# Performance work log

Measured on AMD Instinct MI355X. Metric: run time of the kernel, lower is better.

The kernel has to match this reference:

```python
import jax, jax.numpy as jnp
import numpy as np

B, C, Lc, Vc = 16, 8, 30, 10000
Lp, Vp = 64, 2000
N_IV = 128
BETA_C = 0.7
BETA_P = 0.7


def setup_inputs() -> dict:
    key = jax.random.key(0)
    ks = jax.random.split(key, 9)
    pred_captions = jax.random.normal(ks[0], (B, C, Lc, Vc), jnp.float32)
    gt_captions = jax.random.randint(ks[1], (B, C, Lc), 0, Vc)
    gt_cap_lens = jax.random.randint(ks[2], (B, C), 1, Lc + 1).astype(jnp.int32)
    gt_caps_count = jax.random.randint(ks[3], (B,), 1, C + 1).astype(jnp.int32)
    pred_program = jax.random.normal(ks[4], (B, Lp, Vp), jnp.float32)
    gt_program = jax.random.randint(ks[5], (B, Lp), 0, Vp)
    gt_prog_len = jax.random.randint(ks[6], (B,), 1, Lp + 1).astype(jnp.int32)
    # intervals [N,2,1]: sort along dim 1 so end >= start (well-conditioned union)
    pred_intervals = jnp.sort(jax.random.uniform(ks[7], (N_IV, 2, 1), jnp.float32), axis=1)
    gt_intervals = jnp.sort(jax.random.uniform(ks[8], (N_IV, 2, 1), jnp.float32), axis=1)
    scores = jnp.ones((3,), jnp.float32)  # config.combination_scores
    return dict(gt_captions=gt_captions, gt_cap_lens=gt_cap_lens,
                pred_captions=pred_captions, gt_program=gt_program,
                gt_prog_len=gt_prog_len, pred_program=pred_program,
                gt_intervals=gt_intervals, pred_intervals=pred_intervals,
                gt_caps_count=gt_caps_count, scores=scores)


def _sentlen_loss(logits, targets, lens, item_mask, beta):
    """SentenceLengthLoss ('mean'): -sum_t logsoftmax[t, tgt_t] / len_i**beta, / n_items.
    logits [..., T, V]; targets [..., T] int; lens [...] int; item_mask [...] bool.
    Masked form is exactly equivalent to the torch ragged gather/concat packing.
    """
    T = logits.shape[-2]
    tok_mask = (jnp.arange(T) < lens[..., None]) & item_mask[..., None]  # [..., T]
    logp = jax.nn.log_softmax(logits, axis=-1)
    tok_lp = jnp.take_along_axis(logp, targets[..., None], axis=-1)[..., 0]  # [..., T]
    w = jnp.where(item_mask,
                  1.0 / jnp.maximum(lens, 1).astype(jnp.float32) ** beta,
                  0.0)  # per-sentence weight 1/len**beta
    loss_sum = -jnp.sum(w[..., None] * jnp.where(tok_mask, tok_lp, 0.0))
    n_items = jnp.sum(item_mask.astype(jnp.float32))
    return loss_sum / n_items


def _iou_loss(pred_iv, gt_iv):
    # pred_iv, gt_iv: [N, 2, 1] (start, end)
    p0, p1 = pred_iv[:, 0, 0], pred_iv[:, 1, 0]
    g0, g1 = gt_iv[:, 0, 0], gt_iv[:, 1, 0]
    inter = jnp.clip(jnp.minimum(p1, g1) - jnp.maximum(p0, g0), 0.0)
    union = jnp.maximum(p1, g1) - jnp.minimum(p0, g0)
    return 1.0 - jnp.sum(inter / union) / pred_iv.shape[0]


def reference(gt_captions, gt_cap_lens, pred_captions, gt_program, gt_prog_len,
              pred_program, gt_intervals, pred_intervals, gt_caps_count, scores):
    # captions: caption i of video j is active iff i < gt_caps_count[j]
    cap_item_mask = jnp.arange(pred_captions.shape[1])[None, :] < gt_caps_count[:, None]
    cap_loss = _sentlen_loss(pred_captions, gt_captions, gt_cap_lens,
                             cap_item_mask, BETA_C)
    # program: one sequence per batch element, all active
    prog_item_mask = jnp.ones((pred_program.shape[0],), bool)
    prog_loss = _sentlen_loss(pred_program, gt_program, gt_prog_len,
                              prog_item_mask, BETA_P)
    iou_loss = _iou_loss(pred_intervals, gt_intervals)
    losses = jnp.stack([cap_loss, prog_loss, iou_loss])
    loss = jnp.sum(scores * losses)
    return (loss, cap_loss, prog_loss, iou_loss)
```

## Files before the change

### kernel.cpp

```cpp
#include <hip/hip_runtime.h>
#include <math.h>

#define B   16
#define C   8
#define LC  30
#define VC  10000
#define LP  64
#define VP  2000
#define N_IV 128
#define BETA 0.7f

constexpr int CAP_ROWS    = B * C * LC;
constexpr int PROG_ROWS   = B * LP;
constexpr int PROG_BLOCKS = PROG_ROWS / 4;
constexpr int N4C = VC / 4;
constexpr int KC  = (N4C + 255) / 256;
constexpr int N4P = VP / 4;
constexpr int KP  = (N4P + 63) / 64;

__global__ __launch_bounds__(256) void rows_kernel(
    const float* __restrict__ pred_cap,  const int* __restrict__ gt_cap,
    const int*  __restrict__ cap_lens,   const int* __restrict__ caps_count,
    const float* __restrict__ pred_prog, const int* __restrict__ gt_prog,
    const int*  __restrict__ prog_len,
    float* __restrict__ cap_part, float* __restrict__ prog_part)
{
    __shared__ float sred[4];
    __shared__ float ssum[4];

    const int bid = blockIdx.x;
    const int tid = threadIdx.x;

    if (bid < CAP_ROWS) {
        const int b   = bid / (C * LC);
        const int rem = bid % (C * LC);
        const int c   = rem / LC;
        const int t   = rem % LC;
        const int len = cap_lens[b * C + c];
        if (c >= caps_count[b] || t >= len) {
            if (tid == 0) cap_part[bid] = 0.0f;
            return;
        }
        const float*  row  = pred_cap + (size_t)bid * VC;
        const float4* row4 = (const float4*)row;

        float4 v[KC];
        #pragma unroll
        for (int k = 0; k < KC; k++) {
            const int j = tid + k * 256;
            if (j < N4C) v[k] = row4[j];
            else v[k] = make_float4(-INFINITY, -INFINITY, -INFINITY, -INFINITY);
        }

        float m = -INFINITY;
        #pragma unroll
        for (int k = 0; k < KC; k++)
            m = fmaxf(m, fmaxf(fmaxf(v[k].x, v[k].y), fmaxf(v[k].z, v[k].w)));
        #pragma unroll
        for (int off = 32; off; off >>= 1) m = fmaxf(m, __shfl_xor(m, off, 64));

        const int wid = tid >> 6;
        if ((tid & 63) == 0) sred[wid] = m;
        __syncthreads();
        const float M = fmaxf(fmaxf(sred[0], sred[1]), fmaxf(sred[2], sred[3]));

        float s = 0.0f;
        #pragma unroll
        for (int k = 0; k < KC; k++)
            s += __expf(v[k].x - M) + __expf(v[k].y - M)
               + __expf(v[k].z - M) + __expf(v[k].w - M);
        #pragma unroll
        for (int off = 32; off; off >>= 1) s += __shfl_xor(s, off, 64);

        if ((tid & 63) == 0) ssum[wid] = s;
        __syncthreads();

        if (tid == 0) {
            const float S   = ssum[0] + ssum[1] + ssum[2] + ssum[3];
            const float lse = M + logf(S);
            const float w   = powf((float)len, -BETA);
            cap_part[bid] = -w * (row[gt_cap[bid]] - lse);
        }
    } else {
        const int pb   = bid - CAP_ROWS;
        const int lane = tid & 63;
        const int wid  = tid >> 6;
        const int r    = pb * 4 + wid;
        const int b    = r / LP;
        const int t    = r % LP;
        const int len  = prog_len[b];
        if (t >= len) {
            if (lane == 0) prog_part[r] = 0.0f;
            return;
        }
        const float*  row  = pred_prog + (size_t)r * VP;
        const float4* row4 = (const float4*)row;

        float4 v[KP];
        #pragma unroll
        for (int k = 0; k < KP; k++) {
            const int j = lane + k * 64;
            if (j < N4P) v[k] = row4[j];
            else v[k] = make_float4(-INFINITY, -INFINITY, -INFINITY, -INFINITY);
        }

        float m = -INFINITY;
        #pragma unroll
        for (int k = 0; k < KP; k++)
            m = fmaxf(m, fmaxf(fmaxf(v[k].x, v[k].y), fmaxf(v[k].z, v[k].w)));
        #pragma unroll
        for (int off = 32; off; off >>= 1) m = fmaxf(m, __shfl_xor(m, off, 64));

        float s = 0.0f;
        #pragma unroll
        for (int k = 0; k < KP; k++)
            s += __expf(v[k].x - m) + __expf(v[k].y - m)
               + __expf(v[k].z - m) + __expf(v[k].w - m);
        #pragma unroll
        for (int off = 32; off; off >>= 1) s += __shfl_xor(s, off, 64);

        if (lane == 0) {
            const float lse = m + logf(s);
            const float w   = powf((float)len, -BETA);
            prog_part[r] = -w * (row[gt_prog[r]] - lse);
        }
    }
}

__device__ inline float wave_sum(float v) {
    #pragma unroll
    for (int off = 32; off; off >>= 1) v += __shfl_xor(v, off, 64);
    return v;
}

__global__ __launch_bounds__(256) void finish_kernel(
    const float* __restrict__ cap_part, const float* __restrict__ prog_part,
    const int*  __restrict__ caps_count,
    const float* __restrict__ pred_iv, const float* __restrict__ gt_iv,
    const float* __restrict__ scores, float* __restrict__ out)
{
    const int tid = threadIdx.x;

    float cs = 0.0f;
    for (int i = tid; i < CAP_ROWS; i += 256) cs += cap_part[i];
    float ps = 0.0f;
    for (int i = tid; i < PROG_ROWS; i += 256) ps += prog_part[i];

    float is = 0.0f;
    if (tid < N_IV) {
        const float p0 = pred_iv[tid * 2 + 0];
        const float p1 = pred_iv[tid * 2 + 1];
        const float g0 = gt_iv[tid * 2 + 0];
        const float g1 = gt_iv[tid * 2 + 1];
        const float inter = fmaxf(fminf(p1, g1) - fmaxf(p0, g0), 0.0f);
        const float uni   = fmaxf(p1, g1) - fminf(p0, g0);
        is = inter / uni;
    }

    float nc = 0.0f;
    if (tid < B) nc = (float)caps_count[tid];

    cs = wave_sum(cs);
    ps = wave_sum(ps);
    is = wave_sum(is);
    nc = wave_sum(nc);

    __shared__ float red[4][4];
    const int wid = tid >> 6;
    if ((tid & 63) == 0) {
        red[0][wid] = cs; red[1][wid] = ps; red[2][wid] = is; red[3][wid] = nc;
    }
    __syncthreads();

    if (tid == 0) {
        const float CS = red[0][0] + red[0][1] + red[0][2] + red[0][3];
        const float PS = red[1][0] + red[1][1] + red[1][2] + red[1][3];
        const float IS = red[2][0] + red[2][1] + red[2][2] + red[2][3];
        const float NC = red[3][0] + red[3][1] + red[3][2] + red[3][3];

        const float cap_loss  = CS / NC;
        const float prog_loss = PS / (float)B;
        const float iou_loss  = 1.0f - IS / (float)N_IV;
        const float loss = scores[0] * cap_loss + scores[1] * prog_loss
                         + scores[2] * iou_loss;
        out[0] = loss;
        out[1] = cap_loss;
        out[2] = prog_loss;
        out[3] = iou_loss;
    }
}

extern "C" void kernel_launch(void* const* d_in, const int* in_sizes, int n_in,
                              void* d_out, int out_size, void* d_ws, size_t ws_size,
                              hipStream_t stream) {
    const int*   gt_captions    = (const int*)  d_in[0];
    const int*   gt_cap_lens    = (const int*)  d_in[1];
    const float* pred_captions  = (const float*)d_in[2];
    const int*   gt_program     = (const int*)  d_in[3];
    const int*   gt_prog_len    = (const int*)  d_in[4];
    const float* pred_program   = (const float*)d_in[5];
    const float* gt_intervals   = (const float*)d_in[6];
    const float* pred_intervals = (const float*)d_in[7];
    const int*   gt_caps_count  = (const int*)  d_in[8];
    const float* scores         = (const float*)d_in[9];
    float* out = (float*)d_out;

    float* cap_part  = (float*)d_ws;
    float* prog_part = cap_part + CAP_ROWS;

    rows_kernel<<<CAP_ROWS + PROG_BLOCKS, 256, 0, stream>>>(
        pred_captions, gt_captions, gt_cap_lens, gt_caps_count,
        pred_program, gt_program, gt_prog_len,
        cap_part, prog_part);

    finish_kernel<<<1, 256, 0, stream>>>(
        cap_part, prog_part, gt_caps_count,
        pred_intervals, gt_intervals, scores, out);
}
```

Before: 22.77 us.

## Split caption rows into per-wave halves and merge partial softmax in finish kernel

Each caption row is now split into two halves, and a single wavefront computes each half's max and sum-exp. This drops the block-level shared-memory reductions and both __syncthreads. The finish kernel merges the two partial (m, s) pairs per row, gathers the target logit, and applies the length weight. The target-logit gather and weight math move into the single-block finish kernel, which adds serial work there. Fast-math __logf/__expf also replace logf/powf.

```diff
diff --git a/kernel.cpp b/kernel.cpp
--- a/kernel.cpp
+++ b/kernel.cpp
@@ -11,91 +11,81 @@
 #define BETA 0.7f
 
 constexpr int CAP_ROWS    = B * C * LC;
+constexpr int CAP_HALVES  = CAP_ROWS * 2;
 constexpr int PROG_ROWS   = B * LP;
+constexpr int CAP_BLOCKS  = CAP_HALVES / 4;
 constexpr int PROG_BLOCKS = PROG_ROWS / 4;
-constexpr int N4C = VC / 4;
-constexpr int KC  = (N4C + 255) / 256;
+constexpr int GRID        = CAP_BLOCKS + PROG_BLOCKS;
+constexpr int N4H = (VC / 2) / 4;
+constexpr int KH  = (N4H + 63) / 64;
 constexpr int N4P = VP / 4;
 constexpr int KP  = (N4P + 63) / 64;
 
 __global__ __launch_bounds__(256) void rows_kernel(
-    const float* __restrict__ pred_cap,  const int* __restrict__ gt_cap,
+    const float* __restrict__ pred_cap,
     const int*  __restrict__ cap_lens,   const int* __restrict__ caps_count,
     const float* __restrict__ pred_prog, const int* __restrict__ gt_prog,
     const int*  __restrict__ prog_len,
-    float* __restrict__ cap_part, float* __restrict__ prog_part)
+    float* __restrict__ cap_m, float* __restrict__ cap_s,
+    float* __restrict__ prog_part)
 {
-    __shared__ float sred[4];
-    __shared__ float ssum[4];
-
-    const int bid = blockIdx.x;
-    const int tid = threadIdx.x;
-
-    if (bid < CAP_ROWS) {
-        const int b   = bid / (C * LC);
-        const int rem = bid % (C * LC);
-        const int c   = rem / LC;
-        const int t   = rem % LC;
-        const int len = cap_lens[b * C + c];
-        if (c >= caps_count[b] || t >= len) {
-            if (tid == 0) cap_part[bid] = 0.0f;
-            return;
-        }
-        const float*  row  = pred_cap + (size_t)bid * VC;
-        const float4* row4 = (const float4*)row;
-
-        float4 v[KC];
-        #pragma unroll
-        for (int k = 0; k < KC; k++) {
-            const int j = tid + k * 256;
-            if (j < N4C) v[k] = row4[j];
+    const int tid  = threadIdx.x;
+    const int lane = tid & 63;
+    const int wid  = tid >> 6;
+    const int bid  = blockIdx.x;
+
+    if (bid < CAP_BLOCKS) {
+        const int h    = bid * 4 + wid;
+        const int row  = h >> 1;
+        const int half = h & 1;
+        const int b    = row / (C * LC);
+        const int rem  = row % (C * LC);
+        const int c    = rem / LC;
+        const int t    = rem % LC;
+        const int len  = cap_lens[b * C + c];
+        if (c >= caps_count[b] || t >= len) return;
+
+        const float4* row4 = (const float4*)(pred_cap + (size_t)row * VC)
+                           + half * N4H;
+        float4 v[KH];
+        #pragma unroll
+        for (int k = 0; k < KH; k++) {
+            const int j = lane + k * 64;
+            if (j < N4H) v[k] = row4[j];
             else v[k] = make_float4(-INFINITY, -INFINITY, -INFINITY, -INFINITY);
         }
 
         float m = -INFINITY;
         #pragma unroll
-        for (int k = 0; k < KC; k++)
+        for (int k = 0; k < KH; k++)
             m = fmaxf(m, fmaxf(fmaxf(v[k].x, v[k].y), fmaxf(v[k].z, v[k].w)));
         #pragma unroll
         for (int off = 32; off; off >>= 1) m = fmaxf(m, __shfl_xor(m, off, 64));
 
-        const int wid = tid >> 6;
-        if ((tid & 63) == 0) sred[wid] = m;
-        __syncthreads();
-        const float M = fmaxf(fmaxf(sred[0], sred[1]), fmaxf(sred[2], sred[3]));
-
         float s = 0.0f;
         #pragma unroll
-        for (int k = 0; k < KC; k++)
-            s += __expf(v[k].x - M) + __expf(v[k].y - M)
-               + __expf(v[k].z - M) + __expf(v[k].w - M);
+        for (int k = 0; k < KH; k++)
+            s += __expf(v[k].x - m) + __expf(v[k].y - m)
+               + __expf(v[k].z - m) + __expf(v[k].w - m);
         #pragma unroll
         for (int off = 32; off; off >>= 1) s += __shfl_xor(s, off, 64);
 
-        if ((tid & 63) == 0) ssum[wid] = s;
-        __syncthreads();
-
-        if (tid == 0) {
-            const float S   = ssum[0] + ssum[1] + ssum[2] + ssum[3];
-            const float lse = M + logf(S);
-            const float w   = powf((float)len, -BETA);
-            cap_part[bid] = -w * (row[gt_cap[bid]] - lse);
-        }
+        if (lane == 0) { cap_m[h] = m; cap_s[h] = s; }
     } else {
-        const int pb   = bid - CAP_ROWS;
-        const int lane = tid & 63;
-        const int wid  = tid >> 6;
-        const int r    = pb * 4 + wid;
-        const int b    = r / LP;
-        const int t    = r % LP;
-        const int len  = prog_len[b];
+        const int pb  = bid - CAP_BLOCKS;
+        const int r   = pb * 4 + wid;
+        const int b   = r / LP;
+        const int t   = r % LP;
+        const int len = prog_len[b];
         if (t >= len) {
             if (lane == 0) prog_part[r] = 0.0f;
             return;
         }
         const float*  row  = pred_prog + (size_t)r * VP;
+        const int   tgt     = gt_prog[r];
+        const float logit_t = row[tgt];
+
         const float4* row4 = (const float4*)row;
-
         float4 v[KP];
         #pragma unroll
         for (int k = 0; k < KP; k++) {
@@ -120,9 +110,9 @@
         for (int off = 32; off; off >>= 1) s += __shfl_xor(s, off, 64);
 
         if (lane == 0) {
-            const float lse = m + logf(s);
-            const float w   = powf((float)len, -BETA);
-            prog_part[r] = -w * (row[gt_prog[r]] - lse);
+            const float lse = m + __logf(s);
+            const float w   = __expf(-BETA * __logf((float)len));
+            prog_part[r] = -w * (logit_t - lse);
         }
     }
 }
@@ -134,17 +124,40 @@
 }
 
 __global__ __launch_bounds__(256) void finish_kernel(
-    const float* __restrict__ cap_part, const float* __restrict__ prog_part,
-    const int*  __restrict__ caps_count,
-    const float* __restrict__ pred_iv, const float* __restrict__ gt_iv,
-    const float* __restrict__ scores, float* __restrict__ out)
+    const float* __restrict__ pred_cap, const int* __restrict__ gt_cap,
+    const int*  __restrict__ cap_lens,  const int* __restrict__ caps_count,
+    const float* __restrict__ cap_m,    const float* __restrict__ cap_s,
+    const float* __restrict__ prog_part,
+    const float* __restrict__ pred_iv,  const float* __restrict__ gt_iv,
+    const float* __restrict__ scores,   float* __restrict__ out)
 {
     const int tid = threadIdx.x;
 
     float cs = 0.0f;
-    for (int i = tid; i < CAP_ROWS; i += 256) cs += cap_part[i];
+    #pragma unroll
+    for (int it = 0; it < CAP_ROWS / 256; ++it) {
+        const int row = tid + it * 256;
+        const int b   = row / (C * LC);
+        const int rem = row % (C * LC);
+        const int c   = rem / LC;
+        const int t   = rem % LC;
+        const int len = cap_lens[b * C + c];
+        if (c < caps_count[b] && t < len) {
+            const float m0 = cap_m[2 * row],     m1 = cap_m[2 * row + 1];
+            const float s0 = cap_s[2 * row],     s1 = cap_s[2 * row + 1];
+            const float M  = fmaxf(m0, m1);
+            const float S  = s0 * __expf(m0 - M) + s1 * __expf(m1 - M);
+            const float lse = M + __logf(S);
+            const float lt  = pred_cap[(size_t)row * VC + gt_cap[row]];
+            const float w   = __expf(-BETA * __logf((float)len));
+            cs += -w * (lt - lse);
+        }
+    }
+
     float ps = 0.0f;
-    for (int i = tid; i < PROG_ROWS; i += 256) ps += prog_part[i];
+    #pragma unroll
+    for (int it = 0; it < PROG_ROWS / 256; ++it)
+        ps += prog_part[tid + it * 256];
 
     float is = 0.0f;
     if (tid < N_IV) {
@@ -205,15 +218,17 @@
     const float* scores         = (const float*)d_in[9];
     float* out = (float*)d_out;
 
-    float* cap_part  = (float*)d_ws;
-    float* prog_part = cap_part + CAP_ROWS;
-
-    rows_kernel<<<CAP_ROWS + PROG_BLOCKS, 256, 0, stream>>>(
+    float* cap_m     = (float*)d_ws;
+    float* cap_s     = cap_m + CAP_HALVES;
+    float* prog_part = cap_s + CAP_HALVES;
+
+    rows_kernel<<<GRID, 256, 0, stream>>>(
+        pred_captions, gt_cap_lens, gt_caps_count,
+        pred_program, gt_program, gt_prog_len,
+        cap_m, cap_s, prog_part);
+
+    finish_kernel<<<1, 256, 0, stream>>>(
         pred_captions, gt_captions, gt_cap_lens, gt_caps_count,
-        pred_program, gt_program, gt_prog_len,
-        cap_part, prog_part);
-
-    finish_kernel<<<1, 256, 0, stream>>>(
-        cap_part, prog_part, gt_caps_count,
+        cap_m, cap_s, prog_part,
         pred_intervals, gt_intervals, scores, out);
 }
```

New measurement: 29.13 us. 27.9% more time.
